# Kernel tuning notes

Hardware: AMD Instinct MI355X
Metric: run time of the kernel (lower is better)

The kernel has to match this reference:

```python
import jax, jax.numpy as jnp
import numpy as np
from jax import lax

C = 256
B, H, W = 8, 48, 48
DN = ('NCHW', 'OIHW', 'NCHW')


def setup_inputs() -> dict:
    key = jax.random.key(0)
    ks = jax.random.split(key, 20)
    s = 0.05
    d = {
        'x': jax.random.normal(ks[0], (B, C, H, W), jnp.float32),
        # 1x1 convs of AnchoredSelfAttention, stored as [out, in] matrices
        'wq': jax.random.normal(ks[1], (C, C), jnp.float32) * s,
        'bq': jnp.zeros((C,), jnp.float32),
        'wk': jax.random.normal(ks[2], (C, C), jnp.float32) * s,
        'bk': jnp.zeros((C,), jnp.float32),
        'wv': jax.random.normal(ks[3], (C, C), jnp.float32) * s,
        'bv': jnp.zeros((C,), jnp.float32),
        'wa': jax.random.normal(ks[4], (C, C), jnp.float32) * s,
        'ba': jnp.zeros((C,), jnp.float32),
        # global branch (squeeze-excite style)
        'g1w': jax.random.normal(ks[5], (C // 8, C), jnp.float32) * s,
        'g1b': jnp.zeros((C // 8,), jnp.float32),
        'g2w': jax.random.normal(ks[6], (C, C // 8), jnp.float32) * s,
        'g2b': jnp.zeros((C,), jnp.float32),
        # spectral branch: (1,7) then (7,1) convs
        's1w': jax.random.normal(ks[7], (C, C, 1, 7), jnp.float32) * s,
        's1b': jnp.zeros((C,), jnp.float32),
        's2w': jax.random.normal(ks[8], (C, C, 7, 1), jnp.float32) * s,
        's2b': jnp.zeros((C,), jnp.float32),
        # local branch: 3x3 conv
        'lw': jax.random.normal(ks[9], (C, C, 3, 3), jnp.float32) * s,
        'lb': jnp.zeros((C,), jnp.float32),
    }
    return d


def _conv1x1(x, w, b):
    # x: [B,C,H,W], w: [O,C] -> [B,O,H,W]
    return jnp.einsum('bchw,oc->bohw', x, w) + b[None, :, None, None]


def _conv(x, w, b, pad):
    y = lax.conv_general_dilated(x, w, (1, 1), pad, dimension_numbers=DN)
    return y + b[None, :, None, None]


def reference(x, wq, bq, wk, bk, wv, bv, wa, ba,
              g1w, g1b, g2w, g2b, s1w, s1b, s2w, s2b, lw, lb):
    b, c, h, w = x.shape
    n = h * w

    # global branch: adaptive avg pool(1) + 2-layer bottleneck + sigmoid
    m = jnp.mean(x, axis=(2, 3))                       # [B,C]
    g = jax.nn.relu(m @ g1w.T + g1b)                   # [B,C/8]
    global_att = jax.nn.sigmoid(g @ g2w.T + g2b)[:, :, None, None]  # [B,C,1,1]

    # spectral branch: (1,7) conv + relu + (7,1) conv + sigmoid
    sb = jax.nn.relu(_conv(x, s1w, s1b, ((0, 0), (3, 3))))
    spectral_att = jax.nn.sigmoid(_conv(sb, s2w, s2b, ((3, 3), (0, 0))))

    # local branch: 3x3 conv + relu
    local_feat = jax.nn.relu(_conv(x, lw, lb, ((1, 1), (1, 1))))

    # anchored self-attention over full spatial grid (N = H*W)
    q = _conv1x1(x, wq, bq).reshape(b, c, n)           # [B,C,N]
    k = _conv1x1(x, wk, bk).reshape(b, c, n)
    v = _conv1x1(x, wv, bv).reshape(b, c, n)
    anchor = _conv1x1(x, wa, ba)
    scores = jnp.einsum('bcq,bck->bqk', q, k)          # [B,N,N]
    attn = jax.nn.softmax(scores, axis=-1)
    attended = jnp.einsum('bqk,bck->bcq', attn, v).reshape(b, c, h, w)
    attended_feat = x + attended + anchor

    return x * global_att + x * spectral_att + local_feat + attended_feat
```

## Files before the change

kernel.cpp:

```cpp
#include <hip/hip_runtime.h>


typedef unsigned short u16;
typedef unsigned int u32;
typedef __attribute__((ext_vector_type(8))) u16 u16x8;
typedef __attribute__((ext_vector_type(4))) float f32x4;
typedef __attribute__((ext_vector_type(4))) float f4;
typedef __attribute__((ext_vector_type(8))) __bf16 bf16x8;

#define DEVINL __device__ __forceinline__

constexpr int C = 256;
constexpr int N = 2304;
constexpr int HW = 48;
constexpr int BSTRIDE = C * N;
constexpr int BN = 8 * N;
constexpr int XPAD_ROWS = 54 * 54;
constexpr int SPAD_ROWS = 54 * 48;

DEVINL u16 f2bf(float f) {
  u32 u = __builtin_bit_cast(u32, f);
  u += 0x7fffu + ((u >> 16) & 1u);
  return (u16)(u >> 16);
}
DEVINL float bf2f(u16 h) {
  u32 u = ((u32)h) << 16;
  return __builtin_bit_cast(float, u);
}
DEVINL u16x8 ld8(const u16* p) { return *reinterpret_cast<const u16x8*>(p); }
DEVINL void st8(u16* p, u16x8 v) { *reinterpret_cast<u16x8*>(p) = v; }
DEVINL f32x4 mfma16(u16x8 a, u16x8 b, f32x4 c) {
  return __builtin_amdgcn_mfma_f32_16x16x32_bf16(
      __builtin_bit_cast(bf16x8, a), __builtin_bit_cast(bf16x8, b), c, 0, 0, 0);
}
DEVINL void gl16(const void* g, void* l) {
  __builtin_amdgcn_global_load_lds(
      (const __attribute__((address_space(1))) u32*)g,
      (__attribute__((address_space(3))) u32*)l, 16, 0, 0);
}

__global__ __launch_bounds__(256) void prep_kernel(
    const float* __restrict__ x,
    const float* __restrict__ wq, const float* __restrict__ wk,
    const float* __restrict__ wv, const float* __restrict__ wa,
    const float* __restrict__ s1w, const float* __restrict__ s2w,
    const float* __restrict__ lw,
    u16* __restrict__ xpad, u16* __restrict__ sbpad,
    u16* __restrict__ wqh, u16* __restrict__ wkh,
    u16* __restrict__ wvb, u16* __restrict__ wab,
    u16* __restrict__ s1rep, u16* __restrict__ s2rep, u16* __restrict__ lwrep,
    float* __restrict__ mb) {
  const int blk = blockIdx.x;
  const int t = threadIdx.x;
  if (blk < 704) {
    const long CX = (long)8 * XPAD_ROWS * C / 8;
    const long CS = (long)8 * SPAD_ROWS * C / 8;
    u16x8 z = {0, 0, 0, 0, 0, 0, 0, 0};
    for (long k = (long)blk * 256 + t; k < CX + CS; k += 704L * 256) {
      if (k < CX) st8(xpad + k * 8, z);
      else st8(sbpad + (k - CX) * 8, z);
    }
  } else if (blk < 960) {
    int base = (blk - 704) * 256 + t;
    wqh[base] = f2bf(wq[base]);
    wkh[base] = f2bf(wk[base]);
    wvb[base] = f2bf(wv[base]);
    wab[base] = f2bf(wa[base]);
    size_t b7 = (size_t)base * 7, b9 = (size_t)base * 9;
#pragma unroll
    for (int tp = 0; tp < 7; ++tp) s1rep[tp * 65536 + base] = f2bf(s1w[b7 + tp]);
#pragma unroll
    for (int tp = 0; tp < 7; ++tp) s2rep[tp * 65536 + base] = f2bf(s2w[b7 + tp]);
#pragma unroll
    for (int tp = 0; tp < 9; ++tp) lwrep[tp * 65536 + base] = f2bf(lw[b9 + tp]);
  } else {
    __shared__ float ws4[4];
    int r0 = (blk - 960) * 2;
#pragma unroll
    for (int rr = 0; rr < 2; ++rr) {
      const float* p = x + (size_t)(r0 + rr) * N;
      float s = 0.f;
      for (int i = t; i < N; i += 256) s += p[i];
#pragma unroll
      for (int off = 32; off >= 1; off >>= 1) s += __shfl_xor(s, off);
      if ((t & 63) == 0) ws4[t >> 6] = s;
      __syncthreads();
      if (t == 0) mb[r0 + rr] = (ws4[0] + ws4[1] + ws4[2] + ws4[3]) * (1.f / N);
      __syncthreads();
    }
  }
}

__global__ __launch_bounds__(256) void split_x_kernel(
    const float* __restrict__ x, u16* __restrict__ xhi,
    u16* __restrict__ xpad) {
  const int b = blockIdx.z;
  const int p0 = blockIdx.x * 64;
  const int c0 = blockIdx.y * 64;
  const int tid = threadIdx.x;
  __shared__ float tile[64][65];
#pragma unroll
  for (int it = 0; it < 4; ++it) {
    int idx = it * 256 + tid;
    int cr = idx >> 4, pc = (idx & 15) * 4;
    f4 v = *reinterpret_cast<const f4*>(&x[((size_t)b * C + c0 + cr) * N + p0 + pc]);
    tile[cr][pc] = v[0];
    tile[cr][pc + 1] = v[1];
    tile[cr][pc + 2] = v[2];
    tile[cr][pc + 3] = v[3];
  }
  __syncthreads();
#pragma unroll
  for (int it = 0; it < 2; ++it) {
    int idx = it * 256 + tid;
    int pr = idx >> 3, cg = (idx & 7) * 8;
    u16x8 h8;
#pragma unroll
    for (int j = 0; j < 8; ++j) h8[j] = f2bf(tile[cg + j][pr]);
    int p = p0 + pr;
    size_t o = ((size_t)b * N + p) * C + c0 + cg;
    st8(xhi + o, h8);
    int hh = p / HW, ww = p - hh * HW;
    size_t op = ((size_t)b * XPAD_ROWS + (size_t)(hh + 3) * 54 + ww + 3) * C + c0 + cg;
    st8(xpad + op, h8);
  }
}

__global__ __launch_bounds__(256) void global_kernel(
    const float* __restrict__ m, const float* __restrict__ g1w,
    const float* __restrict__ g1b, const float* __restrict__ g2w,
    const float* __restrict__ g2b, float* __restrict__ gatt) {
  int b = blockIdx.x, t = threadIdx.x;
  __shared__ float ms[256], hid[32];
  ms[t] = m[b * 256 + t];
  __syncthreads();
  if (t < 32) {
    float s = g1b[t];
    const float* wr = g1w + t * 256;
    for (int c2 = 0; c2 < 256; ++c2) s += ms[c2] * wr[c2];
    hid[t] = fmaxf(s, 0.f);
  }
  __syncthreads();
  float s = g2b[t];
#pragma unroll
  for (int j = 0; j < 32; ++j) s += hid[j] * g2w[t * 32 + j];
  gatt[b * 256 + t] = 1.f / (1.f + __expf(-s));
}

struct OpDesc {
  const u16* Xh;
  const u16* W;
  const float* bias;
  u16* o0;
  int tk;
  int act;
  int outn;
  int opad;
  int ips;
  int idy;
  int iox;
  int s0, s1;
};
struct OpPack {
  OpDesc d[6];
  int chunk;
  int ny;
};

__global__ __launch_bounds__(256, 3) void fused_gemm_kernel(OpPack pk) {
  const int swz = (blockIdx.x & 7) * pk.chunk + (blockIdx.x >> 3);
  const int xt = swz % 18;
  const int rest = swz / 18;
  const int y = rest % pk.ny;
  const int z = rest / pk.ny;
  const OpDesc dd = pk.d[y >> 1];
  const int mbase = xt * 128;
  const int nbase = (y & 1) * 128;
  const int tid = threadIdx.x;
  const int lane = tid & 63;
  const int wid = tid >> 6;
  const int wm = wid >> 1, wn = wid & 1;
  const int tk = dd.tk;

  __shared__ __align__(16) u16 ldsX[128 * 64];
  __shared__ __align__(16) u16 ldsW[128 * 64];

  f32x4 acc[4][4];
#pragma unroll
  for (int m = 0; m < 4; ++m)
#pragma unroll
    for (int n = 0; n < 4; ++n) acc[m][n] = f32x4{0.f, 0.f, 0.f, 0.f};

  size_t xrow[4], wrow[4];
#pragma unroll
  for (int it = 0; it < 4; ++it) {
    int idx = it * 256 + tid;
    int rr = idx >> 3, ss = idx & 7;
    int perm = ss ^ (rr & 7);
    int p = mbase + rr;
    if (tk == 0) {
      xrow[it] = ((size_t)z * N + p) * 512 + (size_t)perm * 16;
    } else {
      int hh = p / HW, ww = p - hh * HW;
      xrow[it] = ((size_t)z * dd.ips + (size_t)(hh + 3) * dd.idy + ww + dd.iox) * 512 +
                 (size_t)perm * 16;
    }
    wrow[it] = ((size_t)(nbase + rr)) * 512 + (size_t)perm * 16;
  }
  int aoff[2][4], boff[2][4];
#pragma unroll
  for (int kk = 0; kk < 2; ++kk) {
    int seg = kk * 4 + (lane >> 4);
#pragma unroll
    for (int m = 0; m < 4; ++m) {
      int ra = wm * 64 + m * 16 + (lane & 15);
      aoff[kk][m] = ra * 64 + ((seg ^ (ra & 7)) << 3);
      int rb = wn * 64 + m * 16 + (lane & 15);
      boff[kk][m] = rb * 64 + ((seg ^ (rb & 7)) << 3);
    }
  }

  auto stage = [&](int tap, int ks) {
    const char* xs = (const char*)dd.Xh;
    const char* wsrc = (const char*)dd.W + (size_t)tap * 131072;
    int tsh = 0;
    if (tk == 1) tsh = tap - 3;
    else if (tk == 2) tsh = (tap - 3) * dd.idy;
    else if (tk == 3) tsh = (tap / 3 - 1) * dd.idy + (tap % 3 - 1);
    const long xadd = (long)tsh * 512 + ks * 128;
    const long wadd = ks * 128;
#pragma unroll
    for (int it = 0; it < 4; ++it) {
      gl16(xs + xrow[it] + xadd, &ldsX[(it * 4 + wid) * 512]);
      gl16(wsrc + wrow[it] + wadd, &ldsW[(it * 4 + wid) * 512]);
    }
  };

  int t0 = dd.s0;
  int cks = t0 & 3;
  int ctap = t0 >> 2;
  stage(ctap, cks);

#pragma unroll 1
  for (int t = dd.s0; t < dd.s1; ++t) {
    __syncthreads();
    const u16* Alds = dd.outn ? ldsW : ldsX;
    const u16* Blds = dd.outn ? ldsX : ldsW;
#pragma unroll
    for (int kk = 0; kk < 2; ++kk) {
      u16x8 af[4], bfr[4];
#pragma unroll
      for (int m = 0; m < 4; ++m) af[m] = ld8(&Alds[aoff[kk][m]]);
#pragma unroll
      for (int n = 0; n < 4; ++n) bfr[n] = ld8(&Blds[boff[kk][n]]);
      __builtin_amdgcn_s_setprio(1);
#pragma unroll
      for (int m = 0; m < 4; ++m)
#pragma unroll
        for (int n = 0; n < 4; ++n)
          acc[m][n] = mfma16(af[m], bfr[n], acc[m][n]);
      __builtin_amdgcn_s_setprio(0);
    }
    __syncthreads();
    if (t + 1 < dd.s1) {
      if (++cks == 4) { cks = 0; ++ctap; }
      stage(ctap, cks);
    }
  }

  const int r4 = (lane >> 4) * 4, cl = lane & 15;
  const size_t xb = (size_t)z * BSTRIDE;
#pragma unroll
  for (int m = 0; m < 4; ++m) {
#pragma unroll
    for (int n = 0; n < 4; ++n) {
#pragma unroll
      for (int i = 0; i < 4; ++i) {
        int lrow = wm * 64 + m * 16 + r4 + i;
        int lcol = wn * 64 + n * 16 + cl;
        int o = dd.outn ? (nbase + lrow) : (nbase + lcol);
        int pos = dd.outn ? (mbase + lcol) : (mbase + lrow);
        float v = acc[m][n][i];
        if (dd.bias) {
          v += dd.bias[o];
          if (dd.act == 1) v = fmaxf(v, 0.f);
          else if (dd.act == 2) v = 1.f / (1.f + __expf(-v));
        }
        size_t oi;
        if (dd.opad) {
          int hh = pos / HW, ww = pos - hh * HW;
          oi = ((size_t)z * SPAD_ROWS + (size_t)(hh + 3) * 48 + ww) * C + o;
        } else {
          oi = xb + (dd.outn ? ((size_t)o * N + pos) : ((size_t)pos * C + o));
        }
        dd.o0[oi] = f2bf(v);
      }
    }
  }
}

__global__ __launch_bounds__(256, 2) void flash_kernel(
    const u16* __restrict__ Qhi, const u16* __restrict__ Khi,
    const u16* __restrict__ Vb, u16* __restrict__ P0, u16* __restrict__ P1,
    u16* __restrict__ P2, u16* __restrict__ P3, float* __restrict__ ML) {
  const int b = blockIdx.y;
  const int split = blockIdx.z;
  const int q0 = blockIdx.x * 64;
  const int tid = threadIdx.x;
  const int lane = tid & 63;
  const int wid = tid >> 6;
  const int qbase = q0 + wid * 16;
  const int bb = b * N;
  const u16* Vp = Vb + (size_t)b * BSTRIDE;

  __shared__ __align__(16) u16 lds_kh[32 * 256];
  __shared__ __align__(16) u16 lds_v[256 * 32];
  __shared__ __align__(16) u16 p_lds[4][16 * 40];

  u16x8 qfh[8];
  {
    size_t base = ((size_t)(bb + qbase + (lane & 15))) * C + (lane >> 4) * 8;
#pragma unroll
    for (int kc = 0; kc < 8; ++kc) qfh[kc] = ld8(Qhi + base + kc * 32);
  }
  const u16x8 ones = {0x3F80, 0x3F80, 0x3F80, 0x3F80,
                      0x3F80, 0x3F80, 0x3F80, 0x3F80};

  f32x4 o_acc[16];
#pragma unroll
  for (int j = 0; j < 16; ++j) o_acc[j] = f32x4{0.f, 0.f, 0.f, 0.f};
  float m_r[4] = {-1e30f, -1e30f, -1e30f, -1e30f};
  f32x4 l_acc = {0.f, 0.f, 0.f, 0.f};

  u16x8 skh[4], sv[4];
  const int kt0 = split * 18;
  auto issue = [&](int kt) {
    const int k0 = kt * 32;
#pragma unroll
    for (int it = 0; it < 4; ++it) {
      int idx = it * 256 + tid;
      int r = idx >> 5, s = idx & 31;
      skh[it] = ld8(Khi + (size_t)(bb + k0 + r) * C + s * 8);
      int c2 = idx >> 2, s2 = idx & 3;
      sv[it] = ld8(Vp + (size_t)c2 * N + k0 + s2 * 8);
    }
  };
  issue(kt0);

#pragma unroll 1
  for (int t2 = 0; t2 < 18; ++t2) {
    __syncthreads();
#pragma unroll
    for (int it = 0; it < 4; ++it) {
      int idx = it * 256 + tid;
      int r = idx >> 5, s = idx & 31;
      st8(&lds_kh[r * 256 + ((s ^ (r & 7)) << 3)], skh[it]);
      int c2 = idx >> 2, s2 = idx & 3;
      st8(&lds_v[c2 * 32 + ((s2 ^ ((c2 >> 1) & 3)) << 3)], sv[it]);
    }
    __syncthreads();
    if (t2 < 17) issue(kt0 + t2 + 1);

    f32x4 sa0 = {0.f, 0.f, 0.f, 0.f}, sa1 = {0.f, 0.f, 0.f, 0.f};
    __builtin_amdgcn_s_setprio(1);
#pragma unroll
    for (int kc = 0; kc < 8; ++kc) {
      int seg = kc * 4 + (lane >> 4);
      int r0 = lane & 15, r1 = 16 + (lane & 15);
      u16x8 b0 = ld8(&lds_kh[r0 * 256 + ((seg ^ (r0 & 7)) << 3)]);
      u16x8 b1 = ld8(&lds_kh[r1 * 256 + ((seg ^ (r1 & 7)) << 3)]);
      sa0 = mfma16(qfh[kc], b0, sa0);
      sa1 = mfma16(qfh[kc], b1, sa1);
    }
    __builtin_amdgcn_s_setprio(0);

    float tm[4];
#pragma unroll
    for (int i = 0; i < 4; ++i) {
      float v = fmaxf(sa0[i], sa1[i]);
      v = fmaxf(v, __shfl_xor(v, 1));
      v = fmaxf(v, __shfl_xor(v, 2));
      v = fmaxf(v, __shfl_xor(v, 4));
      v = fmaxf(v, __shfl_xor(v, 8));
      tm[i] = v;
    }
    bool need = (tm[0] > m_r[0] + 8.f) | (tm[1] > m_r[1] + 8.f) |
                (tm[2] > m_r[2] + 8.f) | (tm[3] > m_r[3] + 8.f);
    if (__any(need)) {
      float sc[4];
#pragma unroll
      for (int i = 0; i < 4; ++i) {
        float mn = fmaxf(m_r[i], tm[i]);
        sc[i] = __expf(m_r[i] - mn);
        m_r[i] = mn;
        l_acc[i] *= sc[i];
      }
#pragma unroll
      for (int j = 0; j < 16; ++j) {
#pragma unroll
        for (int i = 0; i < 4; ++i) o_acc[j][i] *= sc[i];
      }
    }
    u16* pl = p_lds[wid];
#pragma unroll
    for (int i = 0; i < 4; ++i) {
      float p0 = __expf(sa0[i] - m_r[i]);
      float p1 = __expf(sa1[i] - m_r[i]);
      int row = (lane >> 4) * 4 + i;
      pl[row * 40 + (lane & 15)] = f2bf(p0);
      pl[row * 40 + 16 + (lane & 15)] = f2bf(p1);
    }
    u16x8 pa = ld8(&pl[(lane & 15) * 40 + (lane >> 4) * 8]);
    __builtin_amdgcn_s_setprio(1);
    l_acc = mfma16(pa, ones, l_acc);
#pragma unroll
    for (int cf = 0; cf < 16; ++cf) {
      int col = cf * 16 + (lane & 15);
      u16x8 bv = ld8(&lds_v[col * 32 + (((lane >> 4) ^ ((col >> 1) & 3)) << 3)]);
      o_acc[cf] = mfma16(pa, bv, o_acc[cf]);
    }
    __builtin_amdgcn_s_setprio(0);
  }

  float rl[4];
#pragma unroll
  for (int i = 0; i < 4; ++i) rl[i] = 1.f / l_acc[i];
  u16* Pout = (split == 0) ? P0 : (split == 1) ? P1 : (split == 2) ? P2 : P3;
#pragma unroll
  for (int cf = 0; cf < 16; ++cf) {
#pragma unroll
    for (int i = 0; i < 4; ++i) {
      int q = qbase + (lane >> 4) * 4 + i;
      int c2 = cf * 16 + (lane & 15);
      Pout[(size_t)(bb + q) * C + c2] = f2bf(o_acc[cf][i] * rl[i]);
    }
  }
  if ((lane & 15) == 0) {
#pragma unroll
    for (int i = 0; i < 4; ++i) {
      int q = qbase + (lane >> 4) * 4 + i;
      ML[split * BN + bb + q] = m_r[i];
      ML[(4 + split) * BN + bb + q] = l_acc[i];
    }
  }
}

__global__ __launch_bounds__(256) void compose_kernel(
    const float* __restrict__ x, const float* __restrict__ gatt,
    const u16* __restrict__ sp0, const u16* __restrict__ sp1,
    const float* __restrict__ s2b, const u16* __restrict__ localT,
    const u16* __restrict__ anchT, const u16* __restrict__ P0,
    const u16* __restrict__ P1, const u16* __restrict__ P2,
    const u16* __restrict__ P3, const float* __restrict__ ML,
    float* __restrict__ out) {
  const int b = blockIdx.y;
  const int p0 = blockIdx.x * 32;
  const int t = threadIdx.x;
  const int bb = b * N;
  __shared__ __align__(16) u16 lsA[32 * 72], lsL[32 * 72], lsO[32 * 72];
  __shared__ float aw[4][32];
  if (t < 32) {
    int gq = bb + p0 + t;
    float m0 = ML[gq], m1 = ML[BN + gq], m2 = ML[2 * BN + gq],
          m3 = ML[3 * BN + gq];
    float M = fmaxf(fmaxf(m0, m1), fmaxf(m2, m3));
    float w0 = ML[4 * BN + gq] * __expf(m0 - M);
    float w1 = ML[5 * BN + gq] * __expf(m1 - M);
    float w2 = ML[6 * BN + gq] * __expf(m2 - M);
    float w3 = ML[7 * BN + gq] * __expf(m3 - M);
    float inv = 1.f / (w0 + w1 + w2 + w3);
    aw[0][t] = w0 * inv;
    aw[1][t] = w1 * inv;
    aw[2][t] = w2 * inv;
    aw[3][t] = w3 * inv;
  }
#pragma unroll 1
  for (int cc = 0; cc < 4; ++cc) {
    const int c0 = cc * 64;
    __syncthreads();
    {
      int r = t >> 3, s = t & 7;
      size_t g = (size_t)(bb + p0 + r) * C + c0 + s * 8;
      u16x8 q0 = ld8(sp0 + g), q1 = ld8(sp1 + g), sa8;
#pragma unroll
      for (int j = 0; j < 8; ++j) {
        float v = bf2f(q0[j]) + bf2f(q1[j]) + s2b[c0 + s * 8 + j];
        sa8[j] = f2bf(1.f / (1.f + __expf(-v)));
      }
      st8(&lsA[r * 72 + s * 8], sa8);
      st8(&lsL[r * 72 + s * 8], ld8(localT + g));
      u16x8 a0 = ld8(P0 + g), a1 = ld8(P1 + g), a2 = ld8(P2 + g),
            a3 = ld8(P3 + g), an = ld8(anchT + g);
      float w0 = aw[0][r], w1 = aw[1][r], w2 = aw[2][r], w3 = aw[3][r];
      u16x8 om;
#pragma unroll
      for (int j = 0; j < 8; ++j)
        om[j] = f2bf(w0 * bf2f(a0[j]) + w1 * bf2f(a1[j]) + w2 * bf2f(a2[j]) +
                     w3 * bf2f(a3[j]) + bf2f(an[j]));
      st8(&lsO[r * 72 + s * 8], om);
    }
    __syncthreads();
    int pl = t & 31, cg = t >> 5;
    int p = p0 + pl;
#pragma unroll
    for (int j = 0; j < 8; ++j) {
      int c2 = c0 + cg * 8 + j;
      size_t xi = ((size_t)b * C + c2) * N + p;
      float xv = x[xi];
      float sa = bf2f(lsA[pl * 72 + (c2 - c0)]);
      float lf = bf2f(lsL[pl * 72 + (c2 - c0)]);
      float om = bf2f(lsO[pl * 72 + (c2 - c0)]);
      float ga = gatt[b * 256 + c2];
      out[xi] = xv * (1.f + ga + sa) + lf + om;
    }
  }
}

extern "C" void kernel_launch(void* const* d_in, const int* in_sizes, int n_in,
                              void* d_out, int out_size, void* d_ws,
                              size_t ws_size, hipStream_t stream) {
  (void)in_sizes; (void)n_in; (void)out_size; (void)ws_size;
  const float* x   = (const float*)d_in[0];
  const float* wq  = (const float*)d_in[1];
  const float* bq  = (const float*)d_in[2];
  const float* wk  = (const float*)d_in[3];
  const float* bk  = (const float*)d_in[4];
  const float* wv  = (const float*)d_in[5];
  const float* bv  = (const float*)d_in[6];
  const float* wa  = (const float*)d_in[7];
  const float* ba  = (const float*)d_in[8];
  const float* g1w = (const float*)d_in[9];
  const float* g1b = (const float*)d_in[10];
  const float* g2w = (const float*)d_in[11];
  const float* g2b = (const float*)d_in[12];
  const float* s1w = (const float*)d_in[13];
  const float* s1b = (const float*)d_in[14];
  const float* s2w = (const float*)d_in[15];
  const float* s2b = (const float*)d_in[16];
  const float* lw  = (const float*)d_in[17];
  const float* lb  = (const float*)d_in[18];
  float* out = (float*)d_out;

  char* w = (char*)d_ws;
  const size_t SZB = (size_t)8 * N * C * sizeof(u16);
  const size_t SZXP = (size_t)8 * XPAD_ROWS * C * sizeof(u16);
  const size_t SZSP = (size_t)8 * SPAD_ROWS * C * sizeof(u16);
  u16* xhiT   = (u16*)(w + 0 * SZB);
  u16* sp0    = (u16*)(w + 1 * SZB);
  u16* sp1    = (u16*)(w + 2 * SZB);
  u16* qhiT   = (u16*)(w + 3 * SZB);
  u16* khiT   = (u16*)(w + 4 * SZB);
  u16* vbuf   = (u16*)(w + 5 * SZB);
  u16* localT = (u16*)(w + 6 * SZB);
  u16* OTb    = (u16*)(w + 7 * SZB);
  u16* Pf0    = (u16*)(w + 8 * SZB);
  u16* Pf1    = (u16*)(w + 9 * SZB);
  u16* xpad   = (u16*)(w + 10 * SZB);
  u16* sbpad  = (u16*)(w + 10 * SZB + SZXP);
  char* wp = w + 10 * SZB + SZXP + SZSP;
  u16* wqh   = (u16*)(wp + 0);
  u16* wkh   = (u16*)(wp + 131072);
  u16* wvb   = (u16*)(wp + 262144);
  u16* wab   = (u16*)(wp + 393216);
  u16* s1rep = (u16*)(wp + 524288);
  u16* s2rep = (u16*)(wp + 1441792);
  u16* lwrep = (u16*)(wp + 2359296);
  float* mb    = (float*)(wp + 3538944);
  float* gattb = (float*)(wp + 3547136);
  float* ML    = (float*)(wp + 3555328);

  prep_kernel<<<1984, 256, 0, stream>>>(x, wq, wk, wv, wa, s1w, s2w, lw,
                                        xpad, sbpad, wqh, wkh, wvb, wab,
                                        s1rep, s2rep, lwrep, mb);
  split_x_kernel<<<dim3(36, 4, 8), 256, 0, stream>>>(x, xhiT, xpad);
  global_kernel<<<8, 256, 0, stream>>>(mb, g1w, g1b, g2w, g2b, gattb);

  OpPack pk;
  pk.d[0] = {xpad, lwrep, lb, localT, 3, 1, 0, 0, XPAD_ROWS, 54, 3, 0, 36};
  pk.d[1] = {xpad, s1rep, s1b, sbpad,  1, 1, 0, 1, XPAD_ROWS, 54, 3, 0, 28};
  pk.d[2] = {xhiT, wqh,   bq, qhiT,    0, 0, 0, 0, N, 0, 0, 0, 4};
  pk.d[3] = {xhiT, wkh,   bk, khiT,    0, 0, 0, 0, N, 0, 0, 0, 4};
  pk.d[4] = {xhiT, wvb,   bv, vbuf,    0, 0, 1, 0, N, 0, 0, 0, 4};
  pk.d[5] = {xhiT, wab,   ba, OTb,     0, 0, 0, 0, N, 0, 0, 0, 4};
  pk.chunk = 1728 / 8;
  pk.ny = 12;
  fused_gemm_kernel<<<dim3(1728), 256, 0, stream>>>(pk);

  OpPack pk2;
  pk2.d[0] = {sbpad, s2rep, nullptr, sp0, 2, 0, 0, 0, SPAD_ROWS, 48, 0, 0, 14};
  pk2.d[1] = {sbpad, s2rep, nullptr, sp1, 2, 0, 0, 0, SPAD_ROWS, 48, 0, 14, 28};
  pk2.chunk = 576 / 8;
  pk2.ny = 4;
  fused_gemm_kernel<<<dim3(576), 256, 0, stream>>>(pk2);

  flash_kernel<<<dim3(36, 8, 4), 256, 0, stream>>>(
      qhiT, khiT, vbuf, Pf0, Pf1, xpad, sbpad, ML);

  compose_kernel<<<dim3(72, 8), 256, 0, stream>>>(
      x, gattb, sp0, sp1, s2b, localT, OTb, Pf0, Pf1, xpad, sbpad, ML, out);
}
```

Measured before the change: 251.6 us.

## Double query rows per wave and double-buffer K/V via direct global-to-LDS loads

The flash attention kernel now processes 32 query rows per wave (128 per block) with two sets of accumulators, so each K/V tile staged in LDS feeds twice as many MFMAs. K/V staging switches from register-staged loads plus LDS stores to direct global-to-LDS loads (gl16) into a double buffer, with pre-swizzled source addresses and one barrier per iteration. The grid is halved to 576 blocks, and register pressure roughly doubles (two 16-entry accumulator arrays plus two Q fragment sets), which risks spills or lower occupancy under launch_bounds(256,2).

```diff
diff --git a/kernel.cpp b/kernel.cpp
--- a/kernel.cpp
+++ b/kernel.cpp
@@ -305,126 +305,157 @@
     u16* __restrict__ P2, u16* __restrict__ P3, float* __restrict__ ML) {
   const int b = blockIdx.y;
   const int split = blockIdx.z;
-  const int q0 = blockIdx.x * 64;
+  const int q0 = blockIdx.x * 128;
   const int tid = threadIdx.x;
   const int lane = tid & 63;
   const int wid = tid >> 6;
-  const int qbase = q0 + wid * 16;
+  const int qbase = q0 + wid * 32;
   const int bb = b * N;
   const u16* Vp = Vb + (size_t)b * BSTRIDE;
 
-  __shared__ __align__(16) u16 lds_kh[32 * 256];
-  __shared__ __align__(16) u16 lds_v[256 * 32];
-  __shared__ __align__(16) u16 p_lds[4][16 * 40];
-
-  u16x8 qfh[8];
+  __shared__ __align__(16) u16 lds_k[2][32 * 256];
+  __shared__ __align__(16) u16 lds_v[2][256 * 32];
+  __shared__ __align__(16) u16 p_lds[4][32 * 40];
+
+  u16x8 qf0[8], qf1[8];
   {
-    size_t base = ((size_t)(bb + qbase + (lane & 15))) * C + (lane >> 4) * 8;
-#pragma unroll
-    for (int kc = 0; kc < 8; ++kc) qfh[kc] = ld8(Qhi + base + kc * 32);
+    size_t base0 = ((size_t)(bb + qbase + (lane & 15))) * C + (lane >> 4) * 8;
+    size_t base1 = base0 + (size_t)16 * C;
+#pragma unroll
+    for (int kc = 0; kc < 8; ++kc) {
+      qf0[kc] = ld8(Qhi + base0 + kc * 32);
+      qf1[kc] = ld8(Qhi + base1 + kc * 32);
+    }
   }
   const u16x8 ones = {0x3F80, 0x3F80, 0x3F80, 0x3F80,
                       0x3F80, 0x3F80, 0x3F80, 0x3F80};
 
-  f32x4 o_acc[16];
-#pragma unroll
-  for (int j = 0; j < 16; ++j) o_acc[j] = f32x4{0.f, 0.f, 0.f, 0.f};
-  float m_r[4] = {-1e30f, -1e30f, -1e30f, -1e30f};
-  f32x4 l_acc = {0.f, 0.f, 0.f, 0.f};
-
-  u16x8 skh[4], sv[4];
+  f32x4 o_acc0[16], o_acc1[16];
+#pragma unroll
+  for (int j = 0; j < 16; ++j) {
+    o_acc0[j] = f32x4{0.f, 0.f, 0.f, 0.f};
+    o_acc1[j] = f32x4{0.f, 0.f, 0.f, 0.f};
+  }
+  f32x4 m0 = {-1e30f, -1e30f, -1e30f, -1e30f};
+  f32x4 m1 = {-1e30f, -1e30f, -1e30f, -1e30f};
+  f32x4 l0 = {0.f, 0.f, 0.f, 0.f}, l1 = {0.f, 0.f, 0.f, 0.f};
+
+  const u16* kbase[4];
+  const u16* vbase[4];
+#pragma unroll
+  for (int it = 0; it < 4; ++it) {
+    int slin = (it * 4 + wid) * 64 + lane;
+    int kr = slin >> 5, kc16 = slin & 31;
+    kbase[it] = Khi + (size_t)(bb + kr) * C + ((kc16 ^ (kr & 7)) << 3);
+    int c2 = slin >> 2, s2 = slin & 3;
+    vbase[it] = Vp + (size_t)c2 * N + ((s2 ^ ((c2 >> 1) & 3)) << 3);
+  }
   const int kt0 = split * 18;
-  auto issue = [&](int kt) {
-    const int k0 = kt * 32;
+  auto stage = [&](int buf, int kt) {
 #pragma unroll
     for (int it = 0; it < 4; ++it) {
-      int idx = it * 256 + tid;
-      int r = idx >> 5, s = idx & 31;
-      skh[it] = ld8(Khi + (size_t)(bb + k0 + r) * C + s * 8);
-      int c2 = idx >> 2, s2 = idx & 3;
-      sv[it] = ld8(Vp + (size_t)c2 * N + k0 + s2 * 8);
+      gl16(kbase[it] + (size_t)kt * (32 * C), &lds_k[buf][(it * 4 + wid) * 512]);
+      gl16(vbase[it] + (size_t)kt * 32, &lds_v[buf][(it * 4 + wid) * 512]);
     }
   };
-  issue(kt0);
+
+  stage(0, kt0);
+  __syncthreads();
+  int cur = 0;
 
 #pragma unroll 1
   for (int t2 = 0; t2 < 18; ++t2) {
-    __syncthreads();
-#pragma unroll
-    for (int it = 0; it < 4; ++it) {
-      int idx = it * 256 + tid;
-      int r = idx >> 5, s = idx & 31;
-      st8(&lds_kh[r * 256 + ((s ^ (r & 7)) << 3)], skh[it]);
-      int c2 = idx >> 2, s2 = idx & 3;
-      st8(&lds_v[c2 * 32 + ((s2 ^ ((c2 >> 1) & 3)) << 3)], sv[it]);
-    }
-    __syncthreads();
-    if (t2 < 17) issue(kt0 + t2 + 1);
-
-    f32x4 sa0 = {0.f, 0.f, 0.f, 0.f}, sa1 = {0.f, 0.f, 0.f, 0.f};
+    if (t2 < 17) stage(cur ^ 1, kt0 + t2 + 1);
+
+    const u16* kl = lds_k[cur];
+    f32x4 sa00 = {0.f, 0.f, 0.f, 0.f}, sa01 = {0.f, 0.f, 0.f, 0.f};
+    f32x4 sa10 = {0.f, 0.f, 0.f, 0.f}, sa11 = {0.f, 0.f, 0.f, 0.f};
     __builtin_amdgcn_s_setprio(1);
 #pragma unroll
     for (int kc = 0; kc < 8; ++kc) {
       int seg = kc * 4 + (lane >> 4);
       int r0 = lane & 15, r1 = 16 + (lane & 15);
-      u16x8 b0 = ld8(&lds_kh[r0 * 256 + ((seg ^ (r0 & 7)) << 3)]);
-      u16x8 b1 = ld8(&lds_kh[r1 * 256 + ((seg ^ (r1 & 7)) << 3)]);
-      sa0 = mfma16(qfh[kc], b0, sa0);
-      sa1 = mfma16(qfh[kc], b1, sa1);
+      u16x8 b0 = ld8(&kl[r0 * 256 + ((seg ^ (r0 & 7)) << 3)]);
+      u16x8 b1 = ld8(&kl[r1 * 256 + ((seg ^ (r1 & 7)) << 3)]);
+      sa00 = mfma16(qf0[kc], b0, sa00);
+      sa01 = mfma16(qf0[kc], b1, sa01);
+      sa10 = mfma16(qf1[kc], b0, sa10);
+      sa11 = mfma16(qf1[kc], b1, sa11);
     }
     __builtin_amdgcn_s_setprio(0);
 
-    float tm[4];
+    f32x4 tm0, tm1;
 #pragma unroll
     for (int i = 0; i < 4; ++i) {
-      float v = fmaxf(sa0[i], sa1[i]);
+      float v = fmaxf(sa00[i], sa01[i]);
       v = fmaxf(v, __shfl_xor(v, 1));
       v = fmaxf(v, __shfl_xor(v, 2));
       v = fmaxf(v, __shfl_xor(v, 4));
       v = fmaxf(v, __shfl_xor(v, 8));
-      tm[i] = v;
-    }
-    bool need = (tm[0] > m_r[0] + 8.f) | (tm[1] > m_r[1] + 8.f) |
-                (tm[2] > m_r[2] + 8.f) | (tm[3] > m_r[3] + 8.f);
+      tm0[i] = v;
+      float u = fmaxf(sa10[i], sa11[i]);
+      u = fmaxf(u, __shfl_xor(u, 1));
+      u = fmaxf(u, __shfl_xor(u, 2));
+      u = fmaxf(u, __shfl_xor(u, 4));
+      u = fmaxf(u, __shfl_xor(u, 8));
+      tm1[i] = u;
+    }
+    bool need = false;
+#pragma unroll
+    for (int i = 0; i < 4; ++i)
+      need |= (tm0[i] > m0[i] + 8.f) | (tm1[i] > m1[i] + 8.f);
     if (__any(need)) {
-      float sc[4];
 #pragma unroll
       for (int i = 0; i < 4; ++i) {
-        float mn = fmaxf(m_r[i], tm[i]);
-        sc[i] = __expf(m_r[i] - mn);
-        m_r[i] = mn;
-        l_acc[i] *= sc[i];
+        float mn0 = fmaxf(m0[i], tm0[i]);
+        float sc0 = __expf(m0[i] - mn0);
+        m0[i] = mn0;
+        l0[i] *= sc0;
+        float mn1 = fmaxf(m1[i], tm1[i]);
+        float sc1 = __expf(m1[i] - mn1);
+        m1[i] = mn1;
+        l1[i] *= sc1;
+#pragma unroll
+        for (int j = 0; j < 16; ++j) {
+          o_acc0[j][i] *= sc0;
+          o_acc1[j][i] *= sc1;
+        }
       }
-#pragma unroll
-      for (int j = 0; j < 16; ++j) {
-#pragma unroll
-        for (int i = 0; i < 4; ++i) o_acc[j][i] *= sc[i];
-      }
     }
     u16* pl = p_lds[wid];
 #pragma unroll
     for (int i = 0; i < 4; ++i) {
-      float p0 = __expf(sa0[i] - m_r[i]);
-      float p1 = __expf(sa1[i] - m_r[i]);
       int row = (lane >> 4) * 4 + i;
-      pl[row * 40 + (lane & 15)] = f2bf(p0);
-      pl[row * 40 + 16 + (lane & 15)] = f2bf(p1);
-    }
-    u16x8 pa = ld8(&pl[(lane & 15) * 40 + (lane >> 4) * 8]);
+      pl[row * 40 + (lane & 15)] = f2bf(__expf(sa00[i] - m0[i]));
+      pl[row * 40 + 16 + (lane & 15)] = f2bf(__expf(sa01[i] - m0[i]));
+      pl[(16 + row) * 40 + (lane & 15)] = f2bf(__expf(sa10[i] - m1[i]));
+      pl[(16 + row) * 40 + 16 + (lane & 15)] = f2bf(__expf(sa11[i] - m1[i]));
+    }
+    u16x8 pa0 = ld8(&pl[(lane & 15) * 40 + (lane >> 4) * 8]);
+    u16x8 pa1 = ld8(&pl[(16 + (lane & 15)) * 40 + (lane >> 4) * 8]);
+    const u16* vl = lds_v[cur];
     __builtin_amdgcn_s_setprio(1);
-    l_acc = mfma16(pa, ones, l_acc);
+    l0 = mfma16(pa0, ones, l0);
+    l1 = mfma16(pa1, ones, l1);
 #pragma unroll
     for (int cf = 0; cf < 16; ++cf) {
       int col = cf * 16 + (lane & 15);
-      u16x8 bv = ld8(&lds_v[col * 32 + (((lane >> 4) ^ ((col >> 1) & 3)) << 3)]);
-      o_acc[cf] = mfma16(pa, bv, o_acc[cf]);
+      u16x8 bv = ld8(&vl[col * 32 + (((lane >> 4) ^ ((col >> 1) & 3)) << 3)]);
+      o_acc0[cf] = mfma16(pa0, bv, o_acc0[cf]);
+      o_acc1[cf] = mfma16(pa1, bv, o_acc1[cf]);
     }
     __builtin_amdgcn_s_setprio(0);
-  }
-
-  float rl[4];
-#pragma unroll
-  for (int i = 0; i < 4; ++i) rl[i] = 1.f / l_acc[i];
+
+    __syncthreads();
+    cur ^= 1;
+  }
+
+  f32x4 rl0, rl1;
+#pragma unroll
+  for (int i = 0; i < 4; ++i) {
+    rl0[i] = 1.f / l0[i];
+    rl1[i] = 1.f / l1[i];
+  }
   u16* Pout = (split == 0) ? P0 : (split == 1) ? P1 : (split == 2) ? P2 : P3;
 #pragma unroll
   for (int cf = 0; cf < 16; ++cf) {
@@ -432,15 +463,18 @@
     for (int i = 0; i < 4; ++i) {
       int q = qbase + (lane >> 4) * 4 + i;
       int c2 = cf * 16 + (lane & 15);
-      Pout[(size_t)(bb + q) * C + c2] = f2bf(o_acc[cf][i] * rl[i]);
+      Pout[(size_t)(bb + q) * C + c2] = f2bf(o_acc0[cf][i] * rl0[i]);
+      Pout[(size_t)(bb + q + 16) * C + c2] = f2bf(o_acc1[cf][i] * rl1[i]);
     }
   }
   if ((lane & 15) == 0) {
 #pragma unroll
     for (int i = 0; i < 4; ++i) {
       int q = qbase + (lane >> 4) * 4 + i;
-      ML[split * BN + bb + q] = m_r[i];
-      ML[(4 + split) * BN + bb + q] = l_acc[i];
+      ML[split * BN + bb + q] = m0[i];
+      ML[(4 + split) * BN + bb + q] = l0[i];
+      ML[split * BN + bb + q + 16] = m1[i];
+      ML[(4 + split) * BN + bb + q + 16] = l1[i];
     }
   }
 }
@@ -593,7 +627,7 @@
   pk2.ny = 4;
   fused_gemm_kernel<<<dim3(576), 256, 0, stream>>>(pk2);
 
-  flash_kernel<<<dim3(36, 8, 4), 256, 0, stream>>>(
+  flash_kernel<<<dim3(18, 8, 4), 256, 0, stream>>>(
       qhiT, khiT, vbuf, Pf0, Pf1, xpad, sbpad, ML);
 
   compose_kernel<<<dim3(72, 8), 256, 0, stream>>>(
```

Result: slower. 316.6 us (+25.8%).
